# Kernel optimization log

Measured on AMD Instinct MI355X. Metric: run time of the kernel, lower is better.

The kernel has to match this reference:

```python
import jax, jax.numpy as jnp
import numpy as np

NUM_LEVELS = 16
RESOLUTIONS = np.array([16, 18, 20, 22, 25, 27, 30, 34, 38, 42, 47, 52, 58, 64, 72, 80], dtype=np.int32)
OFFSETS = np.concatenate([np.zeros(1, np.int64), np.cumsum(RESOLUTIONS.astype(np.int64) ** 3)]).astype(np.int32)
BATCH = 2
C_IN = 16
C_OUT = 16
K = 3


def setup_inputs() -> dict:
    key = jax.random.key(0)
    k1, k2, k3 = jax.random.split(key, 3)
    n_total = int(OFFSETS[-1])  # 1846083 embeddings across all levels
    inp = jax.random.normal(k1, (BATCH, n_total, C_IN), dtype=jnp.float32)
    weight = 0.1 * jax.random.normal(k2, (NUM_LEVELS, K, K, K, C_IN, C_OUT), dtype=jnp.float32)
    bias = 0.01 * jax.random.uniform(k3, (NUM_LEVELS, C_OUT), dtype=jnp.float32)
    # offsets / resolutions are static int buffers (kept as numpy so they stay
    # concrete under jit, mirroring registered int buffers in the torch module)
    return {"input": inp, "weight": weight, "bias": bias,
            "offsets": OFFSETS, "resolutions": RESOLUTIONS}


def _conv_all_levels(inp, weight, bias, offsets, resolutions):
    # inp: [B, N_total, C_in]; per level l the slice offsets[l]:offsets[l+1]
    # is a dense R_l^3 grid flattened x-fastest (idx = x + y*R + z*R^2).
    B = inp.shape[0]
    dn = ('NDHWC', 'DHWIO', 'NDHWC')
    outs = []
    for l in range(NUM_LEVELS):
        R = int(resolutions[l])
        off = int(offsets[l])
        x = inp[:, off:off + R ** 3, :].reshape(B, R, R, R, C_IN)  # [B,Z,Y,X,Cin]
        y = jax.lax.conv_general_dilated(
            x, weight[l], window_strides=(1, 1, 1), padding='SAME',
            dimension_numbers=dn)  # zero-padded 3x3x3 neighborhood gather
        y = y + bias[l]
        outs.append(y.reshape(B, R ** 3, C_OUT))
    return jnp.concatenate(outs, axis=1)  # [B, N_total, C_out]


def reference(input, weight, bias, offsets, resolutions):
    return _conv_all_levels(input, weight, bias, offsets, resolutions)
```

## Files before the change

### kernel.cpp

```cpp
#include <hip/hip_runtime.h>

#define NLVL 16
#define NTOT 1846083
#define NTILE 8634
#define NBLOCK 2159

typedef float  f32x4  __attribute__((ext_vector_type(4)));
typedef __bf16 bf16x8 __attribute__((ext_vector_type(8)));
typedef __bf16 bf16x4 __attribute__((ext_vector_type(4)));
typedef unsigned int u32;
typedef unsigned int u32x4 __attribute__((ext_vector_type(4)));

__constant__ int c_R[NLVL]   = {16,18,20,22,25,27,30,34,38,42,47,52,58,64,72,80};
__constant__ int c_off[NLVL] = {0,4096,9928,17928,28576,44201,63884,90884,130188,185060,259148,362971,503579,698691,960835,1334083};
__constant__ int c_czy[NLVL] = {8,9,10,11,13,14,15,17,19,21,24,26,29,32,36,40};
__constant__ int c_cx[NLVL]  = {1,2,2,2,2,2,2,3,3,3,3,4,4,4,5,5};
__constant__ int c_base[17]  = {0,2000,3800,4824,5752,6584,7016,7394,7736,8042,8162,8274,8378,8466,8546,8618,8634};

__device__ __align__(16) unsigned short g_bfrag[NLVL*3*5*64*8];

__global__ void prep_bfrag(const float* __restrict__ wgt) {
    int tid = blockIdx.x * 256 + threadIdx.x;
    if (tid >= NLVL*3*5*64) return;
    int lane = tid & 63;
    int p    = (tid >> 6) % 5;
    int d    = (tid / (5*64)) % 3;
    int l    = tid / (3*5*64);
    int quad = lane >> 4, co = lane & 15;
    unsigned short v[8];
#pragma unroll
    for (int j = 0; j < 8; ++j) {
        int k   = quad*8 + j;
        int tip = k >> 4;
        int ci  = k & 15;
        int t2  = 2*p + tip;
        float f = (t2 < 9) ? wgt[((l*27 + d*9 + t2)*16 + ci)*16 + co] : 0.f;
        v[j] = __builtin_bit_cast(unsigned short, (__bf16)f);
    }
    u32x4 pk;
    pk[0] = (u32)v[0] | ((u32)v[1] << 16);
    pk[1] = (u32)v[2] | ((u32)v[3] << 16);
    pk[2] = (u32)v[4] | ((u32)v[5] << 16);
    pk[3] = (u32)v[6] | ((u32)v[7] << 16);
    *(u32x4*)&g_bfrag[(size_t)tid*8] = pk;
}

__global__ __launch_bounds__(256, 3)
void conv_kernel(const float* __restrict__ in,
                 const float* __restrict__ bias,
                 float* __restrict__ out) {
    __shared__ __align__(16) char slab[4*4608];

    const int t    = threadIdx.x;
    const int lane = t & 63;
    const int wv   = t >> 6;

    int bswz;
    {
        const int q = NBLOCK / 8, r = NBLOCK % 8;
        int xcd = blockIdx.x % 8, i = blockIdx.x / 8;
        bswz = (xcd < r ? xcd * (q + 1) : r * (q + 1) + (xcd - r) * q) + i;
    }

    const int tid4 = bswz*4 + wv;
    if (tid4 >= NTILE) return;
    int idx = 0;
#pragma unroll
    for (int i = 1; i < 16; ++i) if (tid4 >= c_base[i]) idx = i;
    const int l = 15 - idx;
    const int R = c_R[l], off = c_off[l], czy = c_czy[l], cx = c_cx[l];

    int local = tid4 - c_base[idx];
    int per_b = czy*cx*cx;
    int bb = local / per_b;         int r1 = local - bb*per_b;
    int zt = r1 / (czy*cx);         int r2 = r1 - zt*(czy*cx);
    int yt = r2 / cx;               int xt = r2 - yt*cx;
    const int z0 = zt*16;
    const int z1 = (z0 + 16 < R) ? z0 + 16 : R;
    const int y0 = yt*2, x0 = xt*16;
    const int steps = z1 - z0 + 2;

    const int quad = lane >> 4;
    const int m    = lane & 15;
    const int qh   = quad >> 1;

    bf16x8 bfr[15];
#pragma unroll
    for (int d = 0; d < 3; ++d)
#pragma unroll
        for (int p = 0; p < 5; ++p)
            bfr[d*5+p] = *(const bf16x8*)&g_bfrag[(size_t)(((l*3 + d)*5 + p)*64 + lane)*8];

    const char* sbase = (const char*)slab + wv*4608;
    const char* arA[5];
    {
        const int T0[5] = {0, 64, 608, 1152, 1216};
        const int T1[5] = {32, 576, 640, 1184, 1216};
        const int ab = m*32 + (quad & 1)*16;
#pragma unroll
        for (int p = 0; p < 5; ++p) arA[p] = sbase + ab + (qh ? T1[p] : T0[p]);
    }
    char* wbase = (char*)slab + wv*4608 + lane*8;

    const int  zsE = R*R*16;
    const u32  zsB = (u32)zsE*4;
    const long gstartE = ((long)bb*NTOT + off)*16;

    u32 cur[5]; bool okk[5];
#pragma unroll
    for (int s = 0; s < 5; ++s) {
        int c = lane + s*64;
        int yp = c/72; int rem = c - yp*72; int xp = rem>>2; int ci4 = (rem&3)<<2;
        int y = y0 + yp - 1, x = x0 + xp - 1;
        okk[s] = (c < 288) && ((unsigned)y < (unsigned)R) && ((unsigned)x < (unsigned)R);
        long e = gstartE + (long)(z0-1)*zsE + ((long)y*R + x)*16 + ci4;
        cur[s] = (u32)(e*4);
    }
    const bool wr4 = (lane < 32);

    const f32x4 z4 = {0,0,0,0};
    f32x4 LA[5], LB[5];

    {
        const bool zrA = (z0 > 0);
#pragma unroll
        for (int s = 0; s < 5; ++s) { f32x4 v = z4; if (zrA && okk[s]) v = *(const f32x4*)((const char*)in + cur[s]); LA[s] = v; }
#pragma unroll
        for (int s = 0; s < 5; ++s) cur[s] += zsB;
#pragma unroll
        for (int s = 0; s < 5; ++s) { f32x4 v = z4; if (okk[s]) v = *(const f32x4*)((const char*)in + cur[s]); LB[s] = v; }
#pragma unroll
        for (int s = 0; s < 5; ++s) cur[s] += zsB;
#pragma unroll
        for (int s = 0; s < 5; ++s) {
            if (s < 4 || wr4) {
                bf16x4 h = {(__bf16)LA[s][0],(__bf16)LA[s][1],(__bf16)LA[s][2],(__bf16)LA[s][3]};
                *(bf16x4*)(wbase + s*512) = h;
            }
        }
    }

    const bool xok = (x0 + m) < R;
    bool ywr[2];
#pragma unroll
    for (int r = 0; r < 2; ++r) ywr[r] = (y0 + r) < R;
    const f32x4 bv4 = *(const f32x4*)(bias + (l << 4) + (quad << 2));

    float* so[2];
#pragma unroll
    for (int r = 0; r < 2; ++r)
        so[r] = out + gstartE + (((long)z0*R + (y0 + r))*(long)R + (x0 + m))*16 + (quad << 2);

    f32x4 acc0[2], acc1[2], acc2[2];
#pragma unroll
    for (int r = 0; r < 2; ++r) { acc0[r] = z4; acc1[r] = z4; acc2[r] = z4; }

    int zl = z0 + 1;

#define BODY(II, PAR, LN, LO, AX, AY, AZ, ENST)                                         \
    {                                                                                   \
        const bool zr = (zl <= z1) && (zl < R);                                         \
        _Pragma("unroll")                                                               \
        for (int s = 0; s < 5; ++s) {                                                   \
            f32x4 v = z4;                                                               \
            if (zr && okk[s]) v = *(const f32x4*)((const char*)in + cur[s]);            \
            LN[s] = v;                                                                  \
        }                                                                               \
        { u32 a_ = zr ? zsB : 0u;                                                       \
          _Pragma("unroll") for (int s = 0; s < 5; ++s) cur[s] += a_; }                 \
        ++zl;                                                                           \
        _Pragma("unroll")                                                               \
        for (int p = 0; p < 5; ++p) {                                                   \
            _Pragma("unroll")                                                           \
            for (int r = 0; r < 2; ++r) {                                               \
                bf16x8 af = *(const bf16x8*)(arA[p] + (PAR)*2304 + r*576);              \
                AX[r] = __builtin_amdgcn_mfma_f32_16x16x32_bf16(bfr[p],    af, AX[r], 0,0,0); \
                AY[r] = __builtin_amdgcn_mfma_f32_16x16x32_bf16(bfr[5+p],  af, AY[r], 0,0,0); \
                AZ[r] = __builtin_amdgcn_mfma_f32_16x16x32_bf16(bfr[10+p], af, AZ[r], 0,0,0); \
            }                                                                           \
        }                                                                               \
        _Pragma("unroll")                                                               \
        for (int s = 0; s < 5; ++s) {                                                   \
            if (s < 4 || wr4) {                                                         \
                bf16x4 h = {(__bf16)LO[s][0],(__bf16)LO[s][1],(__bf16)LO[s][2],(__bf16)LO[s][3]}; \
                *(bf16x4*)(wbase + ((PAR)^1)*2304 + s*512) = h;                         \
            }                                                                           \
        }                                                                               \
        if ((ENST) && (II) < steps) {                                                   \
            _Pragma("unroll")                                                           \
            for (int r = 0; r < 2; ++r) {                                               \
                if (ywr[r] && xok) { f32x4 o_ = AZ[r] + bv4; *(f32x4*)so[r] = o_; }     \
                so[r] += zsE;                                                           \
            }                                                                           \
        }                                                                               \
        _Pragma("unroll")                                                               \
        for (int r = 0; r < 2; ++r) AZ[r] = z4;                                         \
    }

    BODY(0, 0, LA, LB, acc0, acc2, acc1, 0)
    BODY(1, 1, LB, LA, acc1, acc0, acc2, 0)
    BODY(2, 0, LA, LB, acc2, acc1, acc0, 1)
    BODY(3, 1, LB, LA, acc0, acc2, acc1, 1)
    BODY(4, 0, LA, LB, acc1, acc0, acc2, 1)
    BODY(5, 1, LB, LA, acc2, acc1, acc0, 1)
#pragma unroll 1
    for (int i = 6; i < steps; i += 6) {
        BODY(i+0, 0, LA, LB, acc0, acc2, acc1, 1)
        BODY(i+1, 1, LB, LA, acc1, acc0, acc2, 1)
        BODY(i+2, 0, LA, LB, acc2, acc1, acc0, 1)
        BODY(i+3, 1, LB, LA, acc0, acc2, acc1, 1)
        BODY(i+4, 0, LA, LB, acc1, acc0, acc2, 1)
        BODY(i+5, 1, LB, LA, acc2, acc1, acc0, 1)
    }
#undef BODY
}

extern "C" void kernel_launch(void* const* d_in, const int* in_sizes, int n_in,
                              void* d_out, int out_size, void* d_ws, size_t ws_size,
                              hipStream_t stream) {
    const float* inp = (const float*)d_in[0];
    const float* wgt = (const float*)d_in[1];
    const float* bia = (const float*)d_in[2];
    float* out = (float*)d_out;
    prep_bfrag<<<dim3((NLVL*3*5*64 + 255)/256), dim3(256), 0, stream>>>(wgt);
    conv_kernel<<<dim3(NBLOCK), dim3(256), 0, stream>>>(inp, bia, out);
}
```

Measured before the change: 453.9 us.

## Enlarge per-wave tile to eight y-rows and restructure z-plane pipeline

Each wave now covers 8 output rows in y instead of 2. Each input plane slab (10 rows of halo) is therefore loaded once for 8 rows of MFMA work instead of 4 rows per 2, which cuts redundant halo loads. The load pipeline changes from two register buffers (LA/LB) to a single buffer, written to LDS before the next plane's global loads are issued. Stores are shifted so output lags by two planes. The cost is much more register and LDS pressure (48 KB LDS per block, launch bounds reduced to 2 blocks), fewer blocks, and less latency hiding.

Result: slower. 879.2 us (+93.7%).

```diff
diff --git a/kernel.cpp b/kernel.cpp
--- a/kernel.cpp
+++ b/kernel.cpp
@@ -2,8 +2,8 @@
 
 #define NLVL 16
 #define NTOT 1846083
-#define NTILE 8634
-#define NBLOCK 2159
+#define NTILE 2254
+#define NBLOCK 564
 
 typedef float  f32x4  __attribute__((ext_vector_type(4)));
 typedef __bf16 bf16x8 __attribute__((ext_vector_type(8)));
@@ -13,9 +13,9 @@
 
 __constant__ int c_R[NLVL]   = {16,18,20,22,25,27,30,34,38,42,47,52,58,64,72,80};
 __constant__ int c_off[NLVL] = {0,4096,9928,17928,28576,44201,63884,90884,130188,185060,259148,362971,503579,698691,960835,1334083};
-__constant__ int c_czy[NLVL] = {8,9,10,11,13,14,15,17,19,21,24,26,29,32,36,40};
+__constant__ int c_czy[NLVL] = {2,3,3,3,4,4,4,5,5,6,6,7,8,8,9,10};
 __constant__ int c_cx[NLVL]  = {1,2,2,2,2,2,2,3,3,3,3,4,4,4,5,5};
-__constant__ int c_base[17]  = {0,2000,3800,4824,5752,6584,7016,7394,7736,8042,8162,8274,8378,8466,8546,8618,8634};
+__constant__ int c_base[17]  = {0,500,950,1206,1462,1686,1794,1902,1992,2082,2114,2146,2178,2202,2226,2250,2254};
 
 __device__ __align__(16) unsigned short g_bfrag[NLVL*3*5*64*8];
 
@@ -45,11 +45,11 @@
     *(u32x4*)&g_bfrag[(size_t)tid*8] = pk;
 }
 
-__global__ __launch_bounds__(256, 3)
+__global__ __launch_bounds__(256, 2)
 void conv_kernel(const float* __restrict__ in,
                  const float* __restrict__ bias,
                  float* __restrict__ out) {
-    __shared__ __align__(16) char slab[4*4608];
+    __shared__ __align__(16) char slab[4*12288];
 
     const int t    = threadIdx.x;
     const int lane = t & 63;
@@ -77,7 +77,7 @@
     int yt = r2 / cx;               int xt = r2 - yt*cx;
     const int z0 = zt*16;
     const int z1 = (z0 + 16 < R) ? z0 + 16 : R;
-    const int y0 = yt*2, x0 = xt*16;
+    const int y0 = yt*8, x0 = xt*16;
     const int steps = z1 - z0 + 2;
 
     const int quad = lane >> 4;
@@ -91,7 +91,7 @@
         for (int p = 0; p < 5; ++p)
             bfr[d*5+p] = *(const bf16x8*)&g_bfrag[(size_t)(((l*3 + d)*5 + p)*64 + lane)*8];
 
-    const char* sbase = (const char*)slab + wv*4608;
+    const char* sbase = (const char*)slab + wv*12288;
     const char* arA[5];
     {
         const int T0[5] = {0, 64, 608, 1152, 1216};
@@ -100,117 +100,126 @@
 #pragma unroll
         for (int p = 0; p < 5; ++p) arA[p] = sbase + ab + (qh ? T1[p] : T0[p]);
     }
-    char* wbase = (char*)slab + wv*4608 + lane*8;
+    char* wb = (char*)slab + wv*12288 + lane*8;
 
     const int  zsE = R*R*16;
     const u32  zsB = (u32)zsE*4;
     const long gstartE = ((long)bb*NTOT + off)*16;
 
-    u32 cur[5]; bool okk[5];
-#pragma unroll
-    for (int s = 0; s < 5; ++s) {
+    u32 cur[12]; bool okk[12];
+#pragma unroll
+    for (int s = 0; s < 12; ++s) {
         int c = lane + s*64;
         int yp = c/72; int rem = c - yp*72; int xp = rem>>2; int ci4 = (rem&3)<<2;
         int y = y0 + yp - 1, x = x0 + xp - 1;
-        okk[s] = (c < 288) && ((unsigned)y < (unsigned)R) && ((unsigned)x < (unsigned)R);
+        okk[s] = (c < 720) && ((unsigned)y < (unsigned)R) && ((unsigned)x < (unsigned)R);
         long e = gstartE + (long)(z0-1)*zsE + ((long)y*R + x)*16 + ci4;
         cur[s] = (u32)(e*4);
     }
-    const bool wr4 = (lane < 32);
+    const bool wr11 = (lane < 16);
 
     const f32x4 z4 = {0,0,0,0};
-    f32x4 LA[5], LB[5];
+    f32x4 LA[12];
 
     {
         const bool zrA = (z0 > 0);
 #pragma unroll
-        for (int s = 0; s < 5; ++s) { f32x4 v = z4; if (zrA && okk[s]) v = *(const f32x4*)((const char*)in + cur[s]); LA[s] = v; }
-#pragma unroll
-        for (int s = 0; s < 5; ++s) cur[s] += zsB;
-#pragma unroll
-        for (int s = 0; s < 5; ++s) { f32x4 v = z4; if (okk[s]) v = *(const f32x4*)((const char*)in + cur[s]); LB[s] = v; }
-#pragma unroll
-        for (int s = 0; s < 5; ++s) cur[s] += zsB;
-#pragma unroll
-        for (int s = 0; s < 5; ++s) {
-            if (s < 4 || wr4) {
+        for (int s = 0; s < 12; ++s) {
+            f32x4 v = z4;
+            if (zrA && okk[s]) v = *(const f32x4*)((const char*)in + cur[s]);
+            LA[s] = v;
+        }
+#pragma unroll
+        for (int s = 0; s < 12; ++s) cur[s] += zsB;
+#pragma unroll
+        for (int s = 0; s < 12; ++s) {
+            if (s < 11 || wr11) {
                 bf16x4 h = {(__bf16)LA[s][0],(__bf16)LA[s][1],(__bf16)LA[s][2],(__bf16)LA[s][3]};
-                *(bf16x4*)(wbase + s*512) = h;
+                *(bf16x4*)(wb + s*512) = h;
             }
         }
+#pragma unroll
+        for (int s = 0; s < 12; ++s) {
+            f32x4 v = z4;
+            if (okk[s]) v = *(const f32x4*)((const char*)in + cur[s]);
+            LA[s] = v;
+        }
+#pragma unroll
+        for (int s = 0; s < 12; ++s) cur[s] += zsB;
     }
 
     const bool xok = (x0 + m) < R;
-    bool ywr[2];
-#pragma unroll
-    for (int r = 0; r < 2; ++r) ywr[r] = (y0 + r) < R;
+    bool gr[8];
+#pragma unroll
+    for (int r = 0; r < 8; ++r) gr[r] = ((y0 + r) < R) && xok;
     const f32x4 bv4 = *(const f32x4*)(bias + (l << 4) + (quad << 2));
-
-    float* so[2];
-#pragma unroll
-    for (int r = 0; r < 2; ++r)
-        so[r] = out + gstartE + (((long)z0*R + (y0 + r))*(long)R + (x0 + m))*16 + (quad << 2);
-
-    f32x4 acc0[2], acc1[2], acc2[2];
-#pragma unroll
-    for (int r = 0; r < 2; ++r) { acc0[r] = z4; acc1[r] = z4; acc2[r] = z4; }
+    const int rowE = R*16;
+
+    float* so0 = out + gstartE + (((long)(z0-2)*R + y0)*(long)R + (x0 + m))*16 + (quad << 2);
+
+    f32x4 c0[8], c1[8], c2[8];
+#pragma unroll
+    for (int r = 0; r < 8; ++r) { c0[r] = z4; c1[r] = z4; c2[r] = z4; }
 
     int zl = z0 + 1;
 
-#define BODY(II, PAR, LN, LO, AX, AY, AZ, ENST)                                         \
+#define BODY(II, PAR, AX, AY, AZ)                                                       \
     {                                                                                   \
-        const bool zr = (zl <= z1) && (zl < R);                                         \
         _Pragma("unroll")                                                               \
-        for (int s = 0; s < 5; ++s) {                                                   \
-            f32x4 v = z4;                                                               \
-            if (zr && okk[s]) v = *(const f32x4*)((const char*)in + cur[s]);            \
-            LN[s] = v;                                                                  \
-        }                                                                               \
-        { u32 a_ = zr ? zsB : 0u;                                                       \
-          _Pragma("unroll") for (int s = 0; s < 5; ++s) cur[s] += a_; }                 \
-        ++zl;                                                                           \
+        for (int s = 0; s < 12; ++s) {                                                  \
+            if (s < 11 || wr11) {                                                       \
+                bf16x4 h = {(__bf16)LA[s][0],(__bf16)LA[s][1],(__bf16)LA[s][2],(__bf16)LA[s][3]}; \
+                *(bf16x4*)(wb + ((PAR)^1)*6144 + s*512) = h;                            \
+            }                                                                           \
+        }                                                                               \
+        {                                                                               \
+            const bool zr = (zl <= z1) && (zl < R);                                     \
+            _Pragma("unroll")                                                           \
+            for (int s = 0; s < 12; ++s) {                                              \
+                f32x4 v = z4;                                                           \
+                if (zr && okk[s]) v = *(const f32x4*)((const char*)in + cur[s]);        \
+                LA[s] = v;                                                              \
+            }                                                                           \
+            u32 a_ = zr ? zsB : 0u;                                                     \
+            _Pragma("unroll")                                                           \
+            for (int s = 0; s < 12; ++s) cur[s] += a_;                                  \
+            ++zl;                                                                       \
+        }                                                                               \
         _Pragma("unroll")                                                               \
         for (int p = 0; p < 5; ++p) {                                                   \
             _Pragma("unroll")                                                           \
-            for (int r = 0; r < 2; ++r) {                                               \
-                bf16x8 af = *(const bf16x8*)(arA[p] + (PAR)*2304 + r*576);              \
+            for (int r = 0; r < 8; ++r) {                                               \
+                bf16x8 af = *(const bf16x8*)(arA[p] + (PAR)*6144 + r*576);              \
                 AX[r] = __builtin_amdgcn_mfma_f32_16x16x32_bf16(bfr[p],    af, AX[r], 0,0,0); \
                 AY[r] = __builtin_amdgcn_mfma_f32_16x16x32_bf16(bfr[5+p],  af, AY[r], 0,0,0); \
                 AZ[r] = __builtin_amdgcn_mfma_f32_16x16x32_bf16(bfr[10+p], af, AZ[r], 0,0,0); \
             }                                                                           \
         }                                                                               \
+        if ((II) >= 2 && (II) < steps) {                                                \
+            _Pragma("unroll")                                                           \
+            for (int r = 0; r < 8; ++r) {                                               \
+                if (gr[r]) { f32x4 o_ = AZ[r] + bv4; *(f32x4*)(so0 + (long)r*rowE) = o_; } \
+            }                                                                           \
+        }                                                                               \
+        so0 += zsE;                                                                     \
         _Pragma("unroll")                                                               \
-        for (int s = 0; s < 5; ++s) {                                                   \
-            if (s < 4 || wr4) {                                                         \
-                bf16x4 h = {(__bf16)LO[s][0],(__bf16)LO[s][1],(__bf16)LO[s][2],(__bf16)LO[s][3]}; \
-                *(bf16x4*)(wbase + ((PAR)^1)*2304 + s*512) = h;                         \
-            }                                                                           \
-        }                                                                               \
-        if ((ENST) && (II) < steps) {                                                   \
-            _Pragma("unroll")                                                           \
-            for (int r = 0; r < 2; ++r) {                                               \
-                if (ywr[r] && xok) { f32x4 o_ = AZ[r] + bv4; *(f32x4*)so[r] = o_; }     \
-                so[r] += zsE;                                                           \
-            }                                                                           \
-        }                                                                               \
-        _Pragma("unroll")                                                               \
-        for (int r = 0; r < 2; ++r) AZ[r] = z4;                                         \
-    }
-
-    BODY(0, 0, LA, LB, acc0, acc2, acc1, 0)
-    BODY(1, 1, LB, LA, acc1, acc0, acc2, 0)
-    BODY(2, 0, LA, LB, acc2, acc1, acc0, 1)
-    BODY(3, 1, LB, LA, acc0, acc2, acc1, 1)
-    BODY(4, 0, LA, LB, acc1, acc0, acc2, 1)
-    BODY(5, 1, LB, LA, acc2, acc1, acc0, 1)
+        for (int r = 0; r < 8; ++r) AZ[r] = z4;                                         \
+    }
+
+    BODY(0, 0, c0, c1, c2)
+    BODY(1, 1, c2, c0, c1)
+    BODY(2, 0, c1, c2, c0)
+    BODY(3, 1, c0, c1, c2)
+    BODY(4, 0, c2, c0, c1)
+    BODY(5, 1, c1, c2, c0)
 #pragma unroll 1
     for (int i = 6; i < steps; i += 6) {
-        BODY(i+0, 0, LA, LB, acc0, acc2, acc1, 1)
-        BODY(i+1, 1, LB, LA, acc1, acc0, acc2, 1)
-        BODY(i+2, 0, LA, LB, acc2, acc1, acc0, 1)
-        BODY(i+3, 1, LB, LA, acc0, acc2, acc1, 1)
-        BODY(i+4, 0, LA, LB, acc1, acc0, acc2, 1)
-        BODY(i+5, 1, LB, LA, acc2, acc1, acc0, 1)
+        BODY(i+0, 0, c0, c1, c2)
+        BODY(i+1, 1, c2, c0, c1)
+        BODY(i+2, 0, c1, c2, c0)
+        BODY(i+3, 1, c0, c1, c2)
+        BODY(i+4, 0, c2, c0, c1)
+        BODY(i+5, 1, c1, c2, c0)
     }
 #undef BODY
 }
```
